# Kernel tuning notes

Hardware: AMD Instinct MI355X
Metric: run time of the kernel (lower is better)

## Reference

```python
import jax, jax.numpy as jnp
import numpy as np

B, S, D = 1, 2048, 1536
H, HD = 24, 64
WINDOW = 512
N_ANCHORS = 4
THETA = 10000.0


def _rope(x):
    # x: [B, H, S, hd] -- matches torch code applied on (B*H, S, hd) with offset=0
    hd = x.shape[-1]
    inv_freq = 1.0 / (THETA ** (jnp.arange(0, hd, 2, dtype=jnp.float32) / hd))
    t = jnp.arange(x.shape[2], dtype=jnp.float32)
    freqs = jnp.outer(t, inv_freq)                      # [S, hd//2]
    emb = jnp.concatenate([freqs, freqs], axis=-1)      # [S, hd]
    cos, sin = jnp.cos(emb), jnp.sin(emb)
    x_rot = jnp.concatenate([-x[..., hd // 2:], x[..., : hd // 2]], axis=-1)
    return x * cos + x_rot * sin


def setup_inputs() -> dict:
    key = jax.random.key(0)
    kx, km, kq, kk, kv = jax.random.split(key, 5)
    std = 0.02
    return {
        "x": jax.random.normal(kx, (B, S, D), jnp.float32),
        "spike_mask": jax.random.bernoulli(km, 0.5, (B, S)),
        "Wq": jax.random.normal(kq, (D, D), jnp.float32) * std,
        "Wk": jax.random.normal(kk, (D, D), jnp.float32) * std,
        "Wv": jax.random.normal(kv, (D, D), jnp.float32) * std,
    }


def reference(x, spike_mask, Wq, Wk, Wv):
    Bq, Sq, Dd = x.shape
    # QKV projections (nn.Linear, bias=False: y = x @ W.T), split heads -> [B, H, S, hd]
    Q = jnp.einsum('bsd,ed->bse', x, Wq).reshape(Bq, Sq, H, HD).transpose(0, 2, 1, 3)
    K = jnp.einsum('bsd,ed->bse', x, Wk).reshape(Bq, Sq, H, HD).transpose(0, 2, 1, 3)
    V = jnp.einsum('bsd,ed->bse', x, Wv).reshape(Bq, Sq, H, HD).transpose(0, 2, 1, 3)
    Q = _rope(Q)
    K = _rope(K)

    # structured mask: causal & (within window | global anchor columns)
    pos = jnp.arange(Sq)
    dist = pos[:, None] - pos[None, :]
    attn_mask = (dist >= 0) & ((dist <= WINDOW) | (pos[None, :] < N_ANCHORS))  # [S, S]

    full_mask = attn_mask[None, None] & spike_mask[:, None, None, :]  # [B,1,S,S]
    query_has_any_key = jnp.any(full_mask, axis=-1, keepdims=True)    # [B,1,S,1]
    safe_mask = full_mask | ~query_has_any_key

    scale = HD ** -0.5
    scores = jnp.einsum('bhqd,bhkd->bhqk', Q, K) * scale
    weights = jax.nn.softmax(jnp.where(safe_mask, scores, -jnp.inf), axis=-1)
    out = jnp.einsum('bhqk,bhkd->bhqd', weights, V)
    out = jnp.where(query_has_any_key, out, 0.0)

    out = out.transpose(0, 2, 1, 3).reshape(Bq, Sq, Dd)
    return out * spike_mask[..., None].astype(out.dtype)
```

## Files before the change

kernel.cpp:

```cpp
#include <hip/hip_runtime.h>
#include <cstdint>
#include <cstddef>

#define S_LEN   2048
#define D_MODEL 1536
#define NH      24
#define HDIM    64
#define WINDOW  512
#define NANCH   4

typedef __attribute__((ext_vector_type(8))) short short8;
typedef __attribute__((ext_vector_type(4))) float floatx4;

#define ASYNC_COPY16(g, l) \
    __builtin_amdgcn_global_load_lds((const __attribute__((address_space(1))) uint32_t*)(g), \
                                     (__attribute__((address_space(3))) uint32_t*)(l), 16, 0, 0)

static __device__ __forceinline__ ushort f32_to_bf16(float f) {
    uint32_t u = __float_as_uint(f);
    uint32_t r = (u + 0x7FFFu + ((u >> 16) & 1u)) >> 16;
    return (ushort)r;
}

__global__ __launch_bounds__(256) void convert_prep_kernel(
    const float* __restrict__ x,
    const float* __restrict__ wq, const float* __restrict__ wk, const float* __restrict__ wv,
    const uint8_t* __restrict__ raw,
    ushort* __restrict__ xb, ushort* __restrict__ wb,
    float* __restrict__ normf, float* __restrict__ cs,
    int xq4, int wq4) {
    const int which = blockIdx.y;
    if (which == 4) {
        if (blockIdx.x < 256) {
            int idx = blockIdx.x * 256 + threadIdx.x;
            int s = idx >> 5, i = idx & 31;
            float inv_freq = expf(-(float)i * 0.2878231366242557f);
            float c, sn;
            sincosf((float)s * inv_freq, &sn, &c);
            cs[s * 64 + i]      = c;
            cs[s * 64 + 32 + i] = sn;
            return;
        }
        if (blockIdx.x != 256) return;
        __shared__ int sh[2];
        if (threadIdx.x == 0) { sh[0] = 0; sh[1] = 0; }
        __syncthreads();
        int f = 0, nz = 0;
        for (int i = threadIdx.x; i < S_LEN; i += 256) {
            uint8_t b = raw[i];
            if ((i & 3) == 3 && b == 0x3f) f++;
            if ((i & 3) != 0 && b != 0)    nz++;
        }
        if (f)  atomicAdd(&sh[0], f);
        if (nz) atomicAdd(&sh[1], nz);
        __syncthreads();
        const int mode = (sh[0] > 0) ? 2 : ((sh[1] > 0) ? 1 : 0);
        for (int i = threadIdx.x; i < S_LEN; i += 256) {
            int v;
            if (mode == 2)      v = (((const float*)raw)[i] != 0.0f) ? 1 : 0;
            else if (mode == 1) v = raw[i] ? 1 : 0;
            else                v = (((const int*)raw)[i] != 0) ? 1 : 0;
            normf[i] = v ? 1.0f : 0.0f;
        }
        return;
    }
    const size_t w_elems = (size_t)D_MODEL * D_MODEL;
    const float* src; ushort* dst; int n4;
    if (which == 0)      { src = x;  dst = xb;               n4 = xq4; }
    else if (which == 1) { src = wq; dst = wb;               n4 = wq4; }
    else if (which == 2) { src = wk; dst = wb + w_elems;     n4 = wq4; }
    else                 { src = wv; dst = wb + 2 * w_elems; n4 = wq4; }
    int i = blockIdx.x * blockDim.x + threadIdx.x;
    if (i >= n4) return;
    float4 v = ((const float4*)src)[i];
    ushort4 o;
    o.x = f32_to_bf16(v.x);
    o.y = f32_to_bf16(v.y);
    o.z = f32_to_bf16(v.z);
    o.w = f32_to_bf16(v.w);
    ((ushort4*)dst)[i] = o;
}

__global__ __launch_bounds__(512) void gemm_qkv_kernel(
    const ushort* __restrict__ xb,
    const ushort* __restrict__ wb,
    const float*  __restrict__ cs,
    ushort* __restrict__ Qf, ushort* __restrict__ Kf, ushort* __restrict__ Vf)
{
    const int lb  = blockIdx.x;
    const int idx = (lb & 7) * 72 + (lb >> 3);
    const int z   = idx / 192;
    const int rem = idx % 192;
    const int n2  = rem >> 4;
    const int tm  = rem & 15;
    const ushort* W = wb + (size_t)z * (D_MODEL * (size_t)D_MODEL);

    __shared__ __align__(16) char smem[32768];

    const int tid  = threadIdx.x;
    const int wave = tid >> 6;
    const int lane = tid & 63;

    const int scol = ((lane & 3) ^ ((lane >> 3) & 3)) * 8;
    const int srow = wave * 16 + (lane >> 2);
    const ushort* gA = xb + (size_t)(tm * 128 + srow) * D_MODEL + scol;
    const ushort* gB = W  + (size_t)(n2 * 128 + srow) * D_MODEL + scol;

    const int wm = (wave >> 1) * 32;
    const int wn = (wave & 1) * 64;
    const int lrow  = lane & 15;
    const int quad  = lane >> 4;
    const int xq = (quad ^ ((lrow >> 1) & 3)) * 8;

    floatx4 acc[2][4];
#pragma unroll
    for (int i = 0; i < 2; ++i)
#pragma unroll
        for (int j = 0; j < 4; ++j)
            acc[i][j] = (floatx4){0.f, 0.f, 0.f, 0.f};

    auto STAGE = [&](int b, int kt) {
        ushort* l = (ushort*)(smem + b * 16384) + wave * 512;
        const int ko = kt * 32;
        ASYNC_COPY16(gA + ko, l);
        ASYNC_COPY16(gB + ko, l + 4096);
    };

    auto COMPUTE = [&](int b) {
        const ushort* Ah = (const ushort*)(smem + b * 16384);
        const ushort* Bh = Ah + 4096;
        short8 af[2], bf[4];
#pragma unroll
        for (int i = 0; i < 2; ++i) af[i] = *(const short8*)(&Ah[(wm + i * 16 + lrow) * 32 + xq]);
#pragma unroll
        for (int j = 0; j < 4; ++j) bf[j] = *(const short8*)(&Bh[(wn + j * 16 + lrow) * 32 + xq]);
#pragma unroll
        for (int i = 0; i < 2; ++i)
#pragma unroll
            for (int j = 0; j < 4; ++j)
                acc[i][j] = __builtin_amdgcn_mfma_f32_16x16x32_bf16(af[i], bf[j], acc[i][j], 0, 0, 0);
    };

    STAGE(0, 0);
    __syncthreads();

    int cur = 0;
    for (int kt = 0; kt < D_MODEL / 32 - 1; ++kt) {
        STAGE(cur ^ 1, kt + 1);
        COMPUTE(cur);
        __syncthreads();
        cur ^= 1;
    }
    COMPUTE(cur);

    __syncthreads();

    const int r0 = (lane >> 4) * 4;
    const int c0 = lane & 15;
    const int l16  = lane & 15;
    const int h  = n2 * 2 + (wave & 1);
    const int s0 = tm * 128 + wm;

#pragma unroll
    for (int g = 0; g < 2; ++g) {
        if ((wave >> 2) == g) {
            ushort* Lw = (ushort*)(smem + (wave & 3) * 8192);
            if (z < 2) {
                const float qscale = (z == 0) ? 0.18033688011112042f : 1.0f;
                ushort* O = (z == 0) ? Qf : Kf;
#pragma unroll
                for (int i = 0; i < 2; ++i) {
#pragma unroll
                    for (int jj = 0; jj < 2; ++jj) {
                        const int cl = jj * 16 + c0;
#pragma unroll
                        for (int r = 0; r < 4; ++r) {
                            const int row = s0 + i * 16 + r0 + r;
                            const float c  = cs[row * 64 + cl];
                            const float sn = cs[row * 64 + 32 + cl];
                            const float x0 = acc[i][jj][r];
                            const float x1 = acc[i][jj + 2][r];
                            const int rl = i * 16 + r0 + r;
                            Lw[rl * 72 + cl]      = f32_to_bf16((x0 * c - x1 * sn) * qscale);
                            Lw[rl * 72 + cl + 32] = f32_to_bf16((x1 * c + x0 * sn) * qscale);
                        }
                    }
                }
                const int t16base = tm * 8 + (wave >> 1) * 2;
#pragma unroll
                for (int t = 0; t < 2; ++t) {
#pragma unroll
                    for (int p = 0; p < 2; ++p) {
                        uint4 v = *(uint4*)&Lw[(t * 16 + l16) * 72 + p * 32 + quad * 8];
                        *(uint4*)&O[((((size_t)h * 128 + t16base + t) * 2 + p) * 64 + lane) * 8] = v;
                    }
                }
            } else {
#pragma unroll
                for (int i = 0; i < 2; ++i) {
#pragma unroll
                    for (int j = 0; j < 4; ++j) {
                        const int dl = j * 16 + c0;
                        ushort4 o;
                        o.x = f32_to_bf16(acc[i][j][0]);
                        o.y = f32_to_bf16(acc[i][j][1]);
                        o.z = f32_to_bf16(acc[i][j][2]);
                        o.w = f32_to_bf16(acc[i][j][3]);
                        *(ushort4*)&Lw[dl * 40 + i * 16 + r0] = o;
                    }
                }
                const int kc = tm * 4 + (wave >> 1);
#pragma unroll
                for (int j2 = 0; j2 < 4; ++j2) {
                    uint4 v = *(uint4*)&Lw[(j2 * 16 + l16) * 40 + quad * 8];
                    *(uint4*)&Vf[((((size_t)h * 64 + kc) * 4 + j2) * 64 + lane) * 8] = v;
                }
            }
        }
        __syncthreads();
    }
}

__global__ __launch_bounds__(256) void flash_attn_kernel(
    const ushort* __restrict__ Qf,
    const ushort* __restrict__ Kf,
    const ushort* __restrict__ Vf,
    const float* __restrict__ spikef,
    float* __restrict__ out)
{
    const int lb   = blockIdx.x + (blockIdx.y << 7);
    const int h    = (lb & 7) * 3 + ((lb >> 3) >> 7);
    const int qt16 = (lb >> 3) & 127;
    const int qs   = qt16 * 16;
    const int tid  = threadIdx.x;
    const int wid  = tid >> 6;
    const int lane = tid & 63;
    const int quad = lane >> 4;
    const int l16  = lane & 15;

    __shared__ __align__(16) char smem[4 * 4608];
    char* wreg = smem + wid * 4608;
    ushort* Pst = (ushort*)wreg;

    const ushort* Qp = Qf + (((size_t)h * 128 + qt16) * 2) * 512 + lane * 8;
    const short8 qf0 = *(const short8*)(Qp);
    const short8 qf1 = *(const short8*)(Qp + 512);

    const int q_lane = qs + l16;

    float lsum = 0.f;
    floatx4 Oacc[4];
#pragma unroll
    for (int j2 = 0; j2 < 4; ++j2) Oacc[j2] = (floatx4){0.f, 0.f, 0.f, 0.f};

    const int qtt = (qs + 15) >> 6;
    const int lo = (qs > WINDOW ? qs - WINDOW : 0) >> 6;
    const int has_anchor = (lo > 0) ? 1 : 0;
    const int nt = (qtt - lo + 1) + has_anchor;

    const ushort* Kh = Kf + ((size_t)h * 128) * 1024 + lane * 8;
    const ushort* Vh = Vf + ((size_t)h * 64) * 2048 + lane * 8;

    for (int it = wid; it < nt; it += 4) {
        const int t = has_anchor ? (it == 0 ? 0 : lo + it - 1) : it;
        const int mode = (t == qtt) ? 1 : ((has_anchor && t == 0) ? 3 :
                         ((qs + 15 - t * 64 > WINDOW) ? 2 : 0));

        floatx4 S[4];
        float4 sp[4];
#pragma unroll
        for (int f = 0; f < 4; ++f) {
            const int t16 = t * 4 + f;
            const ushort* Kp = Kh + (size_t)t16 * 1024;
            short8 kf0 = *(const short8*)(Kp);
            short8 kf1 = *(const short8*)(Kp + 512);
            sp[f] = *(const float4*)(spikef + t16 * 16 + quad * 4);
            floatx4 a = (floatx4){0.f, 0.f, 0.f, 0.f};
            a = __builtin_amdgcn_mfma_f32_16x16x32_bf16(kf0, qf0, a, 0, 0, 0);
            a = __builtin_amdgcn_mfma_f32_16x16x32_bf16(kf1, qf1, a, 0, 0, 0);
            S[f] = a;
        }

#pragma unroll
        for (int f = 0; f < 4; ++f) {
            const int kb = t * 64 + f * 16 + quad * 4;
#pragma unroll
            for (int r = 0; r < 4; ++r) {
                const int k = kb + r;
                float v;
                if (mode == 0)      v = 1.f;
                else if (mode == 1) v = (k <= q_lane) ? 1.f : 0.f;
                else if (mode == 2) v = ((k >= q_lane - WINDOW) || (k < NANCH)) ? 1.f : 0.f;
                else                v = (k < NANCH) ? 1.f : 0.f;
                const float sv = (r == 0) ? sp[f].x : (r == 1) ? sp[f].y : (r == 2) ? sp[f].z : sp[f].w;
                const float w = exp2f(S[f][r]) * v * sv;
                S[f][r] = w;
                lsum += w;
            }
        }

#pragma unroll
        for (int f = 0; f < 4; ++f) {
            uint32_t p01 = (__float_as_uint(S[f][0]) >> 16) | (__float_as_uint(S[f][1]) & 0xFFFF0000u);
            uint32_t p23 = (__float_as_uint(S[f][2]) >> 16) | (__float_as_uint(S[f][3]) & 0xFFFF0000u);
            uint2 pk; pk.x = p01; pk.y = p23;
            *(uint2*)(Pst + l16 * 72 + f * 16 + quad * 4) = pk;
        }

#pragma unroll
        for (int c = 0; c < 2; ++c) {
            const short8 pA = *(const short8*)(Pst + l16 * 72 + c * 32 + quad * 8);
            const int kc = t * 2 + c;
#pragma unroll
            for (int j2 = 0; j2 < 4; ++j2) {
                const short8 vf = *(const short8*)(Vh + (size_t)kc * 2048 + j2 * 512);
                Oacc[j2] = __builtin_amdgcn_mfma_f32_16x16x32_bf16(pA, vf, Oacc[j2], 0, 0, 0);
            }
        }
    }

#pragma unroll
    for (int j2 = 0; j2 < 4; ++j2)
        *(floatx4*)(wreg + j2 * 1024 + lane * 16) = Oacc[j2];
    *(float*)(wreg + 4096 + lane * 4) = lsum;
    __syncthreads();

    floatx4 Os = (floatx4){0.f, 0.f, 0.f, 0.f};
    float lt = 0.f;
#pragma unroll
    for (int w = 0; w < 4; ++w) {
        Os += *(const floatx4*)(smem + w * 4608 + wid * 1024 + lane * 16);
        lt += *(const float*)(smem + w * 4608 + 4096 + lane * 4);
    }
    lt += __shfl_xor(lt, 16);
    lt += __shfl_xor(lt, 32);

#pragma unroll
    for (int r = 0; r < 4; ++r) {
        const float lr = __int_as_float(__builtin_amdgcn_ds_bpermute((quad * 4 + r) * 4,
                                                                     __float_as_int(lt)));
        const int qrow = qs + quad * 4 + r;
        const float linv = (lr > 0.f && spikef[qrow] != 0.f) ? (1.0f / lr) : 0.f;
        out[(size_t)qrow * D_MODEL + h * HDIM + wid * 16 + l16] = Os[r] * linv;
    }
}

extern "C" void kernel_launch(void* const* d_in, const int* in_sizes, int n_in,
                              void* d_out, int out_size, void* d_ws, size_t ws_size,
                              hipStream_t stream) {
    const float* x     = (const float*)d_in[0];
    const uint8_t* spike_raw = (const uint8_t*)d_in[1];
    const float* Wq    = (const float*)d_in[2];
    const float* Wk    = (const float*)d_in[3];
    const float* Wv    = (const float*)d_in[4];
    float* out = (float*)d_out;

    const size_t xb_elems = (size_t)S_LEN * D_MODEL;
    const size_t w_elems  = (size_t)D_MODEL * D_MODEL;
    const size_t hs_elems = (size_t)NH * S_LEN * HDIM;

    char* ws = (char*)d_ws;
    size_t off = 0;
    ushort* xb = (ushort*)(ws + off); off += xb_elems * 2;
    ushort* wb = (ushort*)(ws + off); off += 3 * w_elems * 2;
    ushort* Qf = (ushort*)(ws + off); off += hs_elems * 2;
    ushort* Kf = (ushort*)(ws + off); off += hs_elems * 2;
    ushort* Vf = (ushort*)(ws + off); off += hs_elems * 2;
    float*  cst = (float*)(ws + off); off += (size_t)S_LEN * 64 * 4;
    float* spike_f = (float*)(ws + off); off += S_LEN * 4;
    if (ws_size < off) return;

    {
        int xq4 = (int)(xb_elems / 4);
        int wq4 = (int)(w_elems / 4);
        convert_prep_kernel<<<dim3(3072, 5), 256, 0, stream>>>(
            x, Wq, Wk, Wv, spike_raw, xb, wb, spike_f, cst, xq4, wq4);
    }

    gemm_qkv_kernel<<<576, 512, 0, stream>>>(xb, wb, cst, Qf, Kf, Vf);

    flash_attn_kernel<<<dim3(128, 24), 256, 0, stream>>>(Qf, Kf, Vf, spike_f, out);
}
```

Before: 171.7 us.

## Fold spike mask into V and MFMA row-sum, pair query tiles per block

The spike mask is now multiplied into V in the GEMM epilogue, and the softmax row sums come from an extra MFMA against a precomputed bf16 spike vector. This removes the per-element spike loads and multiplies and the shuffle reductions in the attention loop. Attention blocks now each handle a short and a long query tile (pr and 127-pr), halving the grid and balancing the causal work. The cost is one extra MFMA per chunk, an extra prep buffer, and a second barrier per half.

```diff
diff --git a/kernel.cpp b/kernel.cpp
--- a/kernel.cpp
+++ b/kernel.cpp
@@ -27,7 +27,7 @@
     const float* __restrict__ wq, const float* __restrict__ wk, const float* __restrict__ wv,
     const uint8_t* __restrict__ raw,
     ushort* __restrict__ xb, ushort* __restrict__ wb,
-    float* __restrict__ normf, float* __restrict__ cs,
+    float* __restrict__ normf, float* __restrict__ cs, ushort* __restrict__ svb,
     int xq4, int wq4) {
     const int which = blockIdx.y;
     if (which == 4) {
@@ -61,6 +61,15 @@
             else if (mode == 1) v = raw[i] ? 1 : 0;
             else                v = (((const int*)raw)[i] != 0) ? 1 : 0;
             normf[i] = v ? 1.0f : 0.0f;
+        }
+        for (int idx = threadIdx.x; idx < 64 * 64 * 8; idx += 256) {
+            int kc = idx >> 9, ln = (idx >> 3) & 63, j = idx & 7;
+            int k = kc * 32 + ((ln >> 4) & 3) * 8 + j;
+            int v;
+            if (mode == 2)      v = (((const float*)raw)[k] != 0.0f) ? 1 : 0;
+            else if (mode == 1) v = raw[k] ? 1 : 0;
+            else                v = (((const int*)raw)[k] != 0) ? 1 : 0;
+            svb[idx] = v ? (ushort)0x3F80 : (ushort)0;
         }
         return;
     }
@@ -85,6 +94,7 @@
     const ushort* __restrict__ xb,
     const ushort* __restrict__ wb,
     const float*  __restrict__ cs,
+    const float*  __restrict__ spikef,
     ushort* __restrict__ Qf, ushort* __restrict__ Kf, ushort* __restrict__ Vf)
 {
     const int lb  = blockIdx.x;
@@ -198,14 +208,15 @@
             } else {
 #pragma unroll
                 for (int i = 0; i < 2; ++i) {
+                    const float4 sp4 = *(const float4*)(spikef + s0 + i * 16 + r0);
 #pragma unroll
                     for (int j = 0; j < 4; ++j) {
                         const int dl = j * 16 + c0;
                         ushort4 o;
-                        o.x = f32_to_bf16(acc[i][j][0]);
-                        o.y = f32_to_bf16(acc[i][j][1]);
-                        o.z = f32_to_bf16(acc[i][j][2]);
-                        o.w = f32_to_bf16(acc[i][j][3]);
+                        o.x = f32_to_bf16(acc[i][j][0] * sp4.x);
+                        o.y = f32_to_bf16(acc[i][j][1] * sp4.y);
+                        o.z = f32_to_bf16(acc[i][j][2] * sp4.z);
+                        o.w = f32_to_bf16(acc[i][j][3] * sp4.w);
                         *(ushort4*)&Lw[dl * 40 + i * 16 + r0] = o;
                     }
                 }
@@ -225,123 +236,124 @@
     const ushort* __restrict__ Qf,
     const ushort* __restrict__ Kf,
     const ushort* __restrict__ Vf,
+    const ushort* __restrict__ svb,
     const float* __restrict__ spikef,
     float* __restrict__ out)
 {
-    const int lb   = blockIdx.x + (blockIdx.y << 7);
-    const int h    = (lb & 7) * 3 + ((lb >> 3) >> 7);
-    const int qt16 = (lb >> 3) & 127;
-    const int qs   = qt16 * 16;
+    const int lb   = blockIdx.x;
+    const int u    = lb >> 3;
+    const int h    = (lb & 7) * 3 + u / 64;
+    const int pr   = u & 63;
     const int tid  = threadIdx.x;
     const int wid  = tid >> 6;
     const int lane = tid & 63;
     const int quad = lane >> 4;
     const int l16  = lane & 15;
 
-    __shared__ __align__(16) char smem[4 * 4608];
-    char* wreg = smem + wid * 4608;
+    __shared__ __align__(16) char smem[4 * 5120];
+    char* wreg = smem + wid * 5120;
     ushort* Pst = (ushort*)wreg;
 
-    const ushort* Qp = Qf + (((size_t)h * 128 + qt16) * 2) * 512 + lane * 8;
-    const short8 qf0 = *(const short8*)(Qp);
-    const short8 qf1 = *(const short8*)(Qp + 512);
-
-    const int q_lane = qs + l16;
-
-    float lsum = 0.f;
-    floatx4 Oacc[4];
-#pragma unroll
-    for (int j2 = 0; j2 < 4; ++j2) Oacc[j2] = (floatx4){0.f, 0.f, 0.f, 0.f};
-
-    const int qtt = (qs + 15) >> 6;
-    const int lo = (qs > WINDOW ? qs - WINDOW : 0) >> 6;
-    const int has_anchor = (lo > 0) ? 1 : 0;
-    const int nt = (qtt - lo + 1) + has_anchor;
-
-    const ushort* Kh = Kf + ((size_t)h * 128) * 1024 + lane * 8;
-    const ushort* Vh = Vf + ((size_t)h * 64) * 2048 + lane * 8;
-
-    for (int it = wid; it < nt; it += 4) {
-        const int t = has_anchor ? (it == 0 ? 0 : lo + it - 1) : it;
-        const int mode = (t == qtt) ? 1 : ((has_anchor && t == 0) ? 3 :
-                         ((qs + 15 - t * 64 > WINDOW) ? 2 : 0));
-
-        floatx4 S[4];
-        float4 sp[4];
-#pragma unroll
-        for (int f = 0; f < 4; ++f) {
-            const int t16 = t * 4 + f;
-            const ushort* Kp = Kh + (size_t)t16 * 1024;
-            short8 kf0 = *(const short8*)(Kp);
-            short8 kf1 = *(const short8*)(Kp + 512);
-            sp[f] = *(const float4*)(spikef + t16 * 16 + quad * 4);
-            floatx4 a = (floatx4){0.f, 0.f, 0.f, 0.f};
-            a = __builtin_amdgcn_mfma_f32_16x16x32_bf16(kf0, qf0, a, 0, 0, 0);
-            a = __builtin_amdgcn_mfma_f32_16x16x32_bf16(kf1, qf1, a, 0, 0, 0);
-            S[f] = a;
-        }
-
-#pragma unroll
-        for (int f = 0; f < 4; ++f) {
-            const int kb = t * 64 + f * 16 + quad * 4;
-#pragma unroll
-            for (int r = 0; r < 4; ++r) {
-                const int k = kb + r;
-                float v;
-                if (mode == 0)      v = 1.f;
-                else if (mode == 1) v = (k <= q_lane) ? 1.f : 0.f;
-                else if (mode == 2) v = ((k >= q_lane - WINDOW) || (k < NANCH)) ? 1.f : 0.f;
-                else                v = (k < NANCH) ? 1.f : 0.f;
-                const float sv = (r == 0) ? sp[f].x : (r == 1) ? sp[f].y : (r == 2) ? sp[f].z : sp[f].w;
-                const float w = exp2f(S[f][r]) * v * sv;
-                S[f][r] = w;
-                lsum += w;
-            }
-        }
-
-#pragma unroll
-        for (int f = 0; f < 4; ++f) {
-            uint32_t p01 = (__float_as_uint(S[f][0]) >> 16) | (__float_as_uint(S[f][1]) & 0xFFFF0000u);
-            uint32_t p23 = (__float_as_uint(S[f][2]) >> 16) | (__float_as_uint(S[f][3]) & 0xFFFF0000u);
-            uint2 pk; pk.x = p01; pk.y = p23;
-            *(uint2*)(Pst + l16 * 72 + f * 16 + quad * 4) = pk;
-        }
-
-#pragma unroll
-        for (int c = 0; c < 2; ++c) {
-            const short8 pA = *(const short8*)(Pst + l16 * 72 + c * 32 + quad * 8);
-            const int kc = t * 2 + c;
-#pragma unroll
-            for (int j2 = 0; j2 < 4; ++j2) {
-                const short8 vf = *(const short8*)(Vh + (size_t)kc * 2048 + j2 * 512);
-                Oacc[j2] = __builtin_amdgcn_mfma_f32_16x16x32_bf16(pA, vf, Oacc[j2], 0, 0, 0);
-            }
-        }
-    }
-
-#pragma unroll
-    for (int j2 = 0; j2 < 4; ++j2)
-        *(floatx4*)(wreg + j2 * 1024 + lane * 16) = Oacc[j2];
-    *(float*)(wreg + 4096 + lane * 4) = lsum;
-    __syncthreads();
-
-    floatx4 Os = (floatx4){0.f, 0.f, 0.f, 0.f};
-    float lt = 0.f;
-#pragma unroll
-    for (int w = 0; w < 4; ++w) {
-        Os += *(const floatx4*)(smem + w * 4608 + wid * 1024 + lane * 16);
-        lt += *(const float*)(smem + w * 4608 + 4096 + lane * 4);
-    }
-    lt += __shfl_xor(lt, 16);
-    lt += __shfl_xor(lt, 32);
-
-#pragma unroll
-    for (int r = 0; r < 4; ++r) {
-        const float lr = __int_as_float(__builtin_amdgcn_ds_bpermute((quad * 4 + r) * 4,
-                                                                     __float_as_int(lt)));
-        const int qrow = qs + quad * 4 + r;
-        const float linv = (lr > 0.f && spikef[qrow] != 0.f) ? (1.0f / lr) : 0.f;
-        out[(size_t)qrow * D_MODEL + h * HDIM + wid * 16 + l16] = Os[r] * linv;
+    const ushort* Kh  = Kf + ((size_t)h * 128) * 1024 + lane * 8;
+    const ushort* Vh  = Vf + ((size_t)h * 64) * 2048 + lane * 8;
+    const ushort* svl = svb + lane * 8;
+
+    for (int half = 0; half < 2; ++half) {
+        const int qt16 = half ? (127 - pr) : pr;
+        const int qs   = qt16 * 16;
+        const int q_lane = qs + l16;
+
+        const ushort* Qp = Qf + (((size_t)h * 128 + qt16) * 2) * 512 + lane * 8;
+        const short8 qf0 = *(const short8*)(Qp);
+        const short8 qf1 = *(const short8*)(Qp + 512);
+
+        floatx4 Oacc[4];
+        floatx4 Lacc = (floatx4){0.f, 0.f, 0.f, 0.f};
+#pragma unroll
+        for (int j2 = 0; j2 < 4; ++j2) Oacc[j2] = (floatx4){0.f, 0.f, 0.f, 0.f};
+
+        const int qtt = (qs + 15) >> 6;
+        const int lo = (qs > WINDOW ? qs - WINDOW : 0) >> 6;
+        const int has_anchor = (lo > 0) ? 1 : 0;
+        const int nt = (qtt - lo + 1) + has_anchor;
+
+        for (int it = wid; it < nt; it += 4) {
+            const int t = has_anchor ? (it == 0 ? 0 : lo + it - 1) : it;
+            const int mode = (t == qtt) ? 1 : ((has_anchor && t == 0) ? 3 :
+                             ((qs + 15 - t * 64 > WINDOW) ? 2 : 0));
+
+            floatx4 S[4];
+#pragma unroll
+            for (int f = 0; f < 4; ++f) {
+                const int t16 = t * 4 + f;
+                const ushort* Kp = Kh + (size_t)t16 * 1024;
+                short8 kf0 = *(const short8*)(Kp);
+                short8 kf1 = *(const short8*)(Kp + 512);
+                floatx4 a = (floatx4){0.f, 0.f, 0.f, 0.f};
+                a = __builtin_amdgcn_mfma_f32_16x16x32_bf16(kf0, qf0, a, 0, 0, 0);
+                a = __builtin_amdgcn_mfma_f32_16x16x32_bf16(kf1, qf1, a, 0, 0, 0);
+                S[f] = a;
+            }
+
+#pragma unroll
+            for (int f = 0; f < 4; ++f) {
+                const int kb = t * 64 + f * 16 + quad * 4;
+#pragma unroll
+                for (int r = 0; r < 4; ++r) {
+                    const int k = kb + r;
+                    const float e = exp2f(S[f][r]);
+                    bool keep;
+                    if (mode == 0)      keep = true;
+                    else if (mode == 1) keep = (k <= q_lane);
+                    else if (mode == 2) keep = ((k >= q_lane - WINDOW) || (k < NANCH));
+                    else                keep = (k < NANCH);
+                    S[f][r] = keep ? e : 0.f;
+                }
+            }
+
+#pragma unroll
+            for (int f = 0; f < 4; ++f) {
+                uint32_t p01 = (__float_as_uint(S[f][0]) >> 16) | (__float_as_uint(S[f][1]) & 0xFFFF0000u);
+                uint32_t p23 = (__float_as_uint(S[f][2]) >> 16) | (__float_as_uint(S[f][3]) & 0xFFFF0000u);
+                uint2 pk; pk.x = p01; pk.y = p23;
+                *(uint2*)(Pst + l16 * 72 + f * 16 + quad * 4) = pk;
+            }
+
+#pragma unroll
+            for (int c = 0; c < 2; ++c) {
+                const short8 pA = *(const short8*)(Pst + l16 * 72 + c * 32 + quad * 8);
+                const int kc = t * 2 + c;
+                const short8 sb = *(const short8*)(svl + (size_t)kc * 512);
+                Lacc = __builtin_amdgcn_mfma_f32_16x16x32_bf16(pA, sb, Lacc, 0, 0, 0);
+#pragma unroll
+                for (int j2 = 0; j2 < 4; ++j2) {
+                    const short8 vf = *(const short8*)(Vh + (size_t)kc * 2048 + j2 * 512);
+                    Oacc[j2] = __builtin_amdgcn_mfma_f32_16x16x32_bf16(pA, vf, Oacc[j2], 0, 0, 0);
+                }
+            }
+        }
+
+#pragma unroll
+        for (int j2 = 0; j2 < 4; ++j2)
+            *(floatx4*)(wreg + j2 * 1024 + lane * 16) = Oacc[j2];
+        *(floatx4*)(wreg + 4096 + lane * 16) = Lacc;
+        __syncthreads();
+
+        floatx4 Os = (floatx4){0.f, 0.f, 0.f, 0.f};
+        floatx4 Lt = (floatx4){0.f, 0.f, 0.f, 0.f};
+#pragma unroll
+        for (int w = 0; w < 4; ++w) {
+            Os += *(const floatx4*)(smem + w * 5120 + wid * 1024 + lane * 16);
+            Lt += *(const floatx4*)(smem + w * 5120 + 4096 + lane * 16);
+        }
+
+#pragma unroll
+        for (int r = 0; r < 4; ++r) {
+            const int qrow = qs + quad * 4 + r;
+            const float linv = (Lt[r] > 0.f && spikef[qrow] != 0.f) ? (1.0f / Lt[r]) : 0.f;
+            out[(size_t)qrow * D_MODEL + h * HDIM + wid * 16 + l16] = Os[r] * linv;
+        }
+        __syncthreads();
     }
 }
 
@@ -368,16 +380,17 @@
     ushort* Vf = (ushort*)(ws + off); off += hs_elems * 2;
     float*  cst = (float*)(ws + off); off += (size_t)S_LEN * 64 * 4;
     float* spike_f = (float*)(ws + off); off += S_LEN * 4;
+    ushort* svb = (ushort*)(ws + off); off += (size_t)64 * 64 * 8 * 2;
     if (ws_size < off) return;
 
     {
         int xq4 = (int)(xb_elems / 4);
         int wq4 = (int)(w_elems / 4);
         convert_prep_kernel<<<dim3(3072, 5), 256, 0, stream>>>(
-            x, Wq, Wk, Wv, spike_raw, xb, wb, spike_f, cst, xq4, wq4);
-    }
-
-    gemm_qkv_kernel<<<576, 512, 0, stream>>>(xb, wb, cst, Qf, Kf, Vf);
-
-    flash_attn_kernel<<<dim3(128, 24), 256, 0, stream>>>(Qf, Kf, Vf, spike_f, out);
-}
+            x, Wq, Wk, Wv, spike_raw, xb, wb, spike_f, cst, svb, xq4, wq4);
+    }
+
+    gemm_qkv_kernel<<<576, 512, 0, stream>>>(xb, wb, cst, spike_f, Qf, Kf, Vf);
+
+    flash_attn_kernel<<<1536, 256, 0, stream>>>(Qf, Kf, Vf, svb, spike_f, out);
+}
```

After: 212.9 us. +24.0%, slower.
